# Kernel tuning notes

Hardware: AMD Instinct MI355X
Metric: run time of the kernel (lower is better)

Reference implementation:

```python
import jax, jax.numpy as jnp
import numpy as np

SEQ, HID, IN, THETA = 4096, 512, 512, 5


def setup_inputs() -> dict:
    key = jax.random.key(0)
    k0, k1, k2, k3, k4 = jax.random.split(key, 5)
    return {
        "input": jax.random.normal(k0, (1, SEQ, IN), jnp.float32),
        "internal": jax.random.normal(k1, (THETA + 1, SEQ, HID), jnp.float32) * 0.1,
        "state": jnp.zeros((1, 1, HID), jnp.float32),
        "W_ih": jax.random.normal(k2, (HID, IN), jnp.float32) / np.sqrt(IN).astype(np.float32),
        "W_hh": jax.random.normal(k3, (HID, HID), jnp.float32) / np.sqrt(HID).astype(np.float32),
        "b": jax.random.normal(k4, (HID,), jnp.float32) * 0.01,
        "theta": THETA,
    }


def reference(input, internal, state, W_ih, W_hh, b, theta):
    # Unbatched path (batched=False), continuousTheta=False, trunc >= seq (no detach).
    # Cell: h' = tanh(x @ W_ih.T + h @ W_hh.T + b + noise); out = h'.
    x = input[0]                      # [S, I]
    pre_x = x @ W_ih.T + b            # [S, H] precompute input drive
    h0 = state[0, 0]                  # [H]

    # Main recurrence over the sequence (theta index 0 of internal drives it).
    def step(h, px_n):
        px, n = px_n
        h_new = jnp.tanh(px + h @ W_hh.T + n)
        return h_new, h_new

    _, hs = jax.lax.scan(step, h0, (pre_x, internal[0]))   # hs: [S, H]

    # Theta rollouts: padded input is zero, so drive = b + noise. The rollout at
    # every timestep starts from that timestep's main state -> vectorize over S
    # and scan over the theta axis.
    def roll(H, n):
        H_new = jnp.tanh(b + H @ W_hh.T + n)
        return H_new, H_new

    _, Hs = jax.lax.scan(roll, hs, internal[1:])           # Hs: [theta, S, H]

    outputs = jnp.concatenate([hs[None], Hs], axis=0)      # [theta+1, S, H]
    final_state = hs[-1][None, None]                        # [1, 1, H]
    return outputs, final_state
```

## Files before the change

### kernel.cpp

```cpp
#include <hip/hip_runtime.h>
#include <cstdint>
#include <cstddef>

#define SEQ 4096
#define HID 512
#define NTHETA 5
#define NBLK 8
#define SENT_BITS 0x40000000u

__device__ __forceinline__ float tanh_fast(float x) {
  x = fminf(fmaxf(x, -20.0f), 20.0f);
  const float e = __expf(2.0f * x);
  return (e - 1.0f) / (e + 1.0f);
}

__device__ __forceinline__ uint4 load_x4_sc1(const unsigned* p) {
  uint4 u;
  asm volatile("global_load_dwordx4 %0, %1, off sc1\n\ts_waitcnt vmcnt(0)"
               : "=v"(u) : "v"(p) : "memory");
  return u;
}

__device__ __forceinline__ float red16(float v) {
  int p;
  p = __builtin_amdgcn_update_dpp(0, __float_as_int(v), 0xB1, 0xF, 0xF, true);
  v += __int_as_float(p);
  p = __builtin_amdgcn_update_dpp(0, __float_as_int(v), 0x4E, 0xF, 0xF, true);
  v += __int_as_float(p);
  v += __int_as_float(__builtin_amdgcn_ds_swizzle(__float_as_int(v), 0x101F));
  p = __builtin_amdgcn_update_dpp(0, __float_as_int(v), 0x128, 0xF, 0xF, true);
  v += __int_as_float(p);
  return v;
}

__device__ __forceinline__ int swz(int f) {
  return (f & ~7) | ((f ^ (f >> 3)) & 7);
}

__global__ __launch_bounds__(256) void gemm_bias_noise(
    const float* __restrict__ A, const float* __restrict__ W,
    const float* __restrict__ bias, const float* __restrict__ noise,
    float* __restrict__ C, int K, int doTanh)
{
  const int N = HID;
  const int bm = blockIdx.y, bn = blockIdx.x;
  const int tid = threadIdx.x;
  const int tx = tid & 15, ty = tid >> 4;
  const int row0 = bm * 64, col0 = bn * 64;
  __shared__ float As[16][68];
  __shared__ float Ws[16][68];
  float acc[4][4] = {{0.f, 0.f, 0.f, 0.f}, {0.f, 0.f, 0.f, 0.f},
                     {0.f, 0.f, 0.f, 0.f}, {0.f, 0.f, 0.f, 0.f}};
  const int lrow = tid >> 2, lkq = tid & 3;
  for (int kt = 0; kt < K; kt += 16) {
    const float4 av = *(const float4*)&A[(size_t)(row0 + lrow) * K + kt + lkq * 4];
    const float4 wv = *(const float4*)&W[(size_t)(col0 + lrow) * K + kt + lkq * 4];
    __syncthreads();
    As[lkq * 4 + 0][lrow] = av.x; As[lkq * 4 + 1][lrow] = av.y;
    As[lkq * 4 + 2][lrow] = av.z; As[lkq * 4 + 3][lrow] = av.w;
    Ws[lkq * 4 + 0][lrow] = wv.x; Ws[lkq * 4 + 1][lrow] = wv.y;
    Ws[lkq * 4 + 2][lrow] = wv.z; Ws[lkq * 4 + 3][lrow] = wv.w;
    __syncthreads();
#pragma unroll
    for (int k = 0; k < 16; ++k) {
      const float4 a = *(const float4*)&As[k][ty * 4];
      const float4 bq = *(const float4*)&Ws[k][tx * 4];
      const float a4[4] = {a.x, a.y, a.z, a.w};
      const float b4[4] = {bq.x, bq.y, bq.z, bq.w};
#pragma unroll
      for (int i = 0; i < 4; ++i)
#pragma unroll
        for (int j = 0; j < 4; ++j)
          acc[i][j] = fmaf(a4[i], b4[j], acc[i][j]);
    }
  }
  const float4 bv = *(const float4*)&bias[col0 + tx * 4];
#pragma unroll
  for (int i = 0; i < 4; ++i) {
    const int row = row0 + ty * 4 + i;
    const float4 nv = *(const float4*)&noise[(size_t)row * N + col0 + tx * 4];
    float4 o;
    o.x = acc[i][0] + bv.x + nv.x;
    o.y = acc[i][1] + bv.y + nv.y;
    o.z = acc[i][2] + bv.z + nv.z;
    o.w = acc[i][3] + bv.w + nv.w;
    if (doTanh) {
      o.x = tanh_fast(o.x); o.y = tanh_fast(o.y);
      o.z = tanh_fast(o.z); o.w = tanh_fast(o.w);
    }
    *(float4*)&C[(size_t)row * N + col0 + tx * 4] = o;
  }
}

__global__ void fill_sentinel(uint4* __restrict__ p, int n4) {
  const int i = blockIdx.x * blockDim.x + threadIdx.x;
  if (i < n4) p[i] = make_uint4(SENT_BITS, SENT_BITS, SENT_BITS, SENT_BITS);
}

__global__ __launch_bounds__(1024) void recurrence(
    const float* __restrict__ Whh, const float* __restrict__ drive,
    const float* __restrict__ h0, unsigned* __restrict__ hexch)
{
  const int blk = blockIdx.x;
  const int base = blk * 64;
  const int tid = threadIdx.x;
  const int i = tid >> 4;
  const int j = tid & 15;
  const int row = base + i;

  __shared__ __align__(16) float hbuf[2][HID];

  float4 wv[8];
#pragma unroll
  for (int c = 0; c < 8; ++c)
    wv[c] = *(const float4*)&Whh[(size_t)row * HID + 32 * j + 4 * c];

  const int ch = (tid < blk * 16) ? tid : tid + 16;
  const int wslot = swz(ch);
  const int zown = swz(row >> 2) * 4 + (row & 3);

  if (tid < HID) {
    hbuf[0][swz(tid >> 2) * 4 + (tid & 3)] = h0[tid];
  }

  for (int t = 0; t < SEQ; ++t) {
    const int buf = t & 1;

    float drv = 0.f;
    if (j == 0) drv = drive[(size_t)t * HID + row];

    if (t > 0 && tid < 112) {
      const unsigned* src = &hexch[(size_t)(t - 1) * HID + 4 * ch];
      uint4 u = load_x4_sc1(src);
      int it = 0;
      while (u.x == SENT_BITS || u.y == SENT_BITS ||
             u.z == SENT_BITS || u.w == SENT_BITS) {
        if ((++it & 7) == 0) {
          u.x = __hip_atomic_load(src + 0, __ATOMIC_RELAXED,
                                  __HIP_MEMORY_SCOPE_AGENT);
          u.y = __hip_atomic_load(src + 1, __ATOMIC_RELAXED,
                                  __HIP_MEMORY_SCOPE_AGENT);
          u.z = __hip_atomic_load(src + 2, __ATOMIC_RELAXED,
                                  __HIP_MEMORY_SCOPE_AGENT);
          u.w = __hip_atomic_load(src + 3, __ATOMIC_RELAXED,
                                  __HIP_MEMORY_SCOPE_AGENT);
        } else {
          u = load_x4_sc1(src);
        }
      }
      ((uint4*)hbuf[buf])[wslot] = u;
    }
    __syncthreads();
    asm volatile("" :: "v"(drv));

    float a0 = 0.f, a1 = 0.f, a2 = 0.f, a3 = 0.f;
#pragma unroll
    for (int c = 0; c < 8; ++c) {
      const float4 h4 = *(const float4*)&hbuf[buf][(8 * j + ((c ^ j) & 7)) * 4];
      a0 = fmaf(wv[c].x, h4.x, a0);
      a1 = fmaf(wv[c].y, h4.y, a1);
      a2 = fmaf(wv[c].z, h4.z, a2);
      a3 = fmaf(wv[c].w, h4.w, a3);
    }
    float sum = (a0 + a1) + (a2 + a3);
    sum = red16(sum);

    if (j == 0) {
      const float y = tanh_fast(sum + drv);
      __hip_atomic_store(&hexch[(size_t)t * HID + row], __float_as_uint(y),
                         __ATOMIC_RELAXED, __HIP_MEMORY_SCOPE_AGENT);
      hbuf[buf ^ 1][zown] = y;
    }
  }
}

__global__ void copy_final(const float* __restrict__ src, float* __restrict__ dst) {
  dst[threadIdx.x] = src[threadIdx.x];
}

extern "C" void kernel_launch(void* const* d_in, const int* in_sizes, int n_in,
                              void* d_out, int out_size, void* d_ws, size_t ws_size,
                              hipStream_t stream) {
  const float* input    = (const float*)d_in[0];
  const float* internal = (const float*)d_in[1];
  const float* state    = (const float*)d_in[2];
  const float* W_ih     = (const float*)d_in[3];
  const float* W_hh     = (const float*)d_in[4];
  const float* bias     = (const float*)d_in[5];
  float* out = (float*)d_out;

  const size_t plane = (size_t)SEQ * HID;
  unsigned* hexch = (unsigned*)out;
  float*    drive = out + 5 * plane;

  fill_sentinel<<<(SEQ * HID / 4 + 255) / 256, 256, 0, stream>>>(
      (uint4*)hexch, SEQ * HID / 4);

  dim3 gg(HID / 64, SEQ / 64);
  gemm_bias_noise<<<gg, 256, 0, stream>>>(input, W_ih, bias, internal, drive,
                                          HID, 0);
  recurrence<<<NBLK, 1024, 0, stream>>>(W_hh, drive, state, hexch);
  for (int k = 0; k < NTHETA; ++k) {
    gemm_bias_noise<<<gg, 256, 0, stream>>>(out + (size_t)k * plane, W_hh, bias,
                                            internal + (size_t)(k + 1) * plane,
                                            out + (size_t)(k + 1) * plane,
                                            HID, 1);
  }
  copy_final<<<1, HID, 0, stream>>>(out + (size_t)4095 * HID, out + 6 * plane);
}
```

Before: 6.745 ms.

## Halve recurrence blocks to 4, each thread computing two hidden rows

The persistent recurrence kernel now runs on 4 workgroups of 128 rows instead of 8 of 64. Each thread holds two W_hh row slices in registers and computes two dot products against the shared hidden state. Results are packed into one 64-bit atomic store. This cuts the number of cross-block exchange participants and the polled chunks per step (96 instead of 112 threads). The cost is doubled register use and FMA work per thread on the sequential critical path.

After: 6.501 ms. 1.04x faster.

```diff
diff --git a/kernel.cpp b/kernel.cpp
--- a/kernel.cpp
+++ b/kernel.cpp
@@ -5,8 +5,11 @@
 #define SEQ 4096
 #define HID 512
 #define NTHETA 5
-#define NBLK 8
+#define NBLK 4
+#define RPB 128
 #define SENT_BITS 0x40000000u
+
+typedef unsigned long long u64;
 
 __device__ __forceinline__ float tanh_fast(float x) {
   x = fminf(fmaxf(x, -20.0f), 20.0f);
@@ -102,34 +105,34 @@
     const float* __restrict__ h0, unsigned* __restrict__ hexch)
 {
   const int blk = blockIdx.x;
-  const int base = blk * 64;
+  const int base = blk * RPB;
   const int tid = threadIdx.x;
   const int i = tid >> 4;
   const int j = tid & 15;
-  const int row = base + i;
+  const int r0 = base + 2 * i;
 
   __shared__ __align__(16) float hbuf[2][HID];
 
-  float4 wv[8];
-#pragma unroll
-  for (int c = 0; c < 8; ++c)
-    wv[c] = *(const float4*)&Whh[(size_t)row * HID + 32 * j + 4 * c];
-
-  const int ch = (tid < blk * 16) ? tid : tid + 16;
+  float4 w0[8], w1[8];
+#pragma unroll
+  for (int c = 0; c < 8; ++c) {
+    w0[c] = *(const float4*)&Whh[(size_t)r0 * HID + 32 * j + 4 * c];
+    w1[c] = *(const float4*)&Whh[(size_t)(r0 + 1) * HID + 32 * j + 4 * c];
+  }
+
+  const int ch = (tid < blk * 32) ? tid : tid + 32;
   const int wslot = swz(ch);
-  const int zown = swz(row >> 2) * 4 + (row & 3);
-
-  if (tid < HID) {
-    hbuf[0][swz(tid >> 2) * 4 + (tid & 3)] = h0[tid];
-  }
+  const int z0 = swz(r0 >> 2) * 4 + (r0 & 3);
+
+  if (tid < HID) hbuf[0][swz(tid >> 2) * 4 + (tid & 3)] = h0[tid];
 
   for (int t = 0; t < SEQ; ++t) {
     const int buf = t & 1;
 
-    float drv = 0.f;
-    if (j == 0) drv = drive[(size_t)t * HID + row];
-
-    if (t > 0 && tid < 112) {
+    float2 dr = make_float2(0.f, 0.f);
+    if (j == 0) dr = *(const float2*)&drive[(size_t)t * HID + r0];
+
+    if (t > 0 && tid < 96) {
       const unsigned* src = &hexch[(size_t)(t - 1) * HID + 4 * ch];
       uint4 u = load_x4_sc1(src);
       int it = 0;
@@ -151,25 +154,32 @@
       ((uint4*)hbuf[buf])[wslot] = u;
     }
     __syncthreads();
-    asm volatile("" :: "v"(drv));
-
-    float a0 = 0.f, a1 = 0.f, a2 = 0.f, a3 = 0.f;
+    asm volatile("" :: "v"(dr.x), "v"(dr.y));
+
+    float a00 = 0.f, a01 = 0.f, a02 = 0.f, a03 = 0.f;
+    float a10 = 0.f, a11 = 0.f, a12 = 0.f, a13 = 0.f;
 #pragma unroll
     for (int c = 0; c < 8; ++c) {
       const float4 h4 = *(const float4*)&hbuf[buf][(8 * j + ((c ^ j) & 7)) * 4];
-      a0 = fmaf(wv[c].x, h4.x, a0);
-      a1 = fmaf(wv[c].y, h4.y, a1);
-      a2 = fmaf(wv[c].z, h4.z, a2);
-      a3 = fmaf(wv[c].w, h4.w, a3);
-    }
-    float sum = (a0 + a1) + (a2 + a3);
-    sum = red16(sum);
+      a00 = fmaf(w0[c].x, h4.x, a00);
+      a01 = fmaf(w0[c].y, h4.y, a01);
+      a02 = fmaf(w0[c].z, h4.z, a02);
+      a03 = fmaf(w0[c].w, h4.w, a03);
+      a10 = fmaf(w1[c].x, h4.x, a10);
+      a11 = fmaf(w1[c].y, h4.y, a11);
+      a12 = fmaf(w1[c].z, h4.z, a12);
+      a13 = fmaf(w1[c].w, h4.w, a13);
+    }
+    float s0 = red16((a00 + a01) + (a02 + a03));
+    float s1 = red16((a10 + a11) + (a12 + a13));
 
     if (j == 0) {
-      const float y = tanh_fast(sum + drv);
-      __hip_atomic_store(&hexch[(size_t)t * HID + row], __float_as_uint(y),
+      const float y0 = tanh_fast(s0 + dr.x);
+      const float y1 = tanh_fast(s1 + dr.y);
+      const u64 pk = (u64)__float_as_uint(y0) | ((u64)__float_as_uint(y1) << 32);
+      __hip_atomic_store((u64*)&hexch[(size_t)t * HID + r0], pk,
                          __ATOMIC_RELAXED, __HIP_MEMORY_SCOPE_AGENT);
-      hbuf[buf ^ 1][zown] = y;
+      *(float2*)&hbuf[buf ^ 1][z0] = make_float2(y0, y1);
     }
   }
 }
```
